# Performance work log

Measured on AMD Instinct MI355X. Metric: run time of the kernel, lower is better.

The kernel has to match this reference:

```python
import jax, jax.numpy as jnp
import numpy as np

N, T, D, H = 8192, 60, 6, 64  # stocks, lookback, d_feat, hidden_size
NEG_SLOPE = 0.01


def setup_inputs() -> dict:
    key = jax.random.key(0)
    ks = jax.random.split(key, 16)
    s = 0.1
    inp = {
        "x": jax.random.normal(ks[0], (N, D * T), jnp.float32),
        # GRU layer 0 (input D -> H), PyTorch gate order [r, z, n]
        "gru_Wih0": jax.random.normal(ks[1], (3 * H, D), jnp.float32) * s,
        "gru_Whh0": jax.random.normal(ks[2], (3 * H, H), jnp.float32) * s,
        "gru_bih0": jax.random.normal(ks[3], (3 * H,), jnp.float32) * s,
        "gru_bhh0": jax.random.normal(ks[4], (3 * H,), jnp.float32) * s,
        # GRU layer 1 (H -> H)
        "gru_Wih1": jax.random.normal(ks[5], (3 * H, H), jnp.float32) * s,
        "gru_Whh1": jax.random.normal(ks[6], (3 * H, H), jnp.float32) * s,
        "gru_bih1": jax.random.normal(ks[7], (3 * H,), jnp.float32) * s,
        "gru_bhh1": jax.random.normal(ks[8], (3 * H,), jnp.float32) * s,
        # attention head
        "transfer_W": jax.random.normal(ks[9], (H, H), jnp.float32) * s,
        "transfer_b": jax.random.normal(ks[10], (H,), jnp.float32) * s,
        "a": jax.random.normal(ks[11], (2 * H, 1), jnp.float32) * s,
        # output head
        "fc_W": jax.random.normal(ks[12], (H, H), jnp.float32) * s,
        "fc_b": jax.random.normal(ks[13], (H,), jnp.float32) * s,
        "out_W": jax.random.normal(ks[14], (1, H), jnp.float32) * s,
        "out_b": jax.random.normal(ks[15], (1,), jnp.float32) * s,
    }
    return inp


def _gru_layer(xs, Wih, Whh, bih, bhh):
    # xs: [T, N, in]; PyTorch GRU cell math, gate order r,z,n
    Hs = Whh.shape[1]

    def step(h, xt):
        gi = xt @ Wih.T + bih
        gh = h @ Whh.T + bhh
        ir, iz, inn = jnp.split(gi, 3, axis=-1)
        hr, hz, hn = jnp.split(gh, 3, axis=-1)
        r = jax.nn.sigmoid(ir + hr)
        z = jax.nn.sigmoid(iz + hz)
        n = jnp.tanh(inn + r * hn)
        h_new = (1.0 - z) * n + z * h
        return h_new, h_new

    h0 = jnp.zeros((xs.shape[1], Hs), xs.dtype)
    _, ys = jax.lax.scan(step, h0, xs)
    return ys  # [T, N, Hs]


def reference(x, gru_Wih0, gru_Whh0, gru_bih0, gru_bhh0,
              gru_Wih1, gru_Whh1, gru_bih1, gru_bhh1,
              transfer_W, transfer_b, a, fc_W, fc_b, out_W, out_b):
    # [N, D*T] -> [N, D, T] -> [T, N, D]
    xs = jnp.transpose(x.reshape(x.shape[0], D, -1), (2, 0, 1))
    ys0 = _gru_layer(xs, gru_Wih0, gru_Whh0, gru_bih0, gru_bhh0)
    ys1 = _gru_layer(ys0, gru_Wih1, gru_Whh1, gru_bih1, gru_bhh1)
    hidden = ys1[-1]  # [N, H] == out[:, -1, :]

    # self_attention: score[k, i] = a[:H].(W x_i) + a[H:].(W x_k)
    t = hidden @ transfer_W.T + transfer_b
    a1 = a[:H, 0]
    a2 = a[H:, 0]
    s1 = t @ a1  # contribution of column index i
    s2 = t @ a2  # contribution of row index k
    scores = jax.nn.leaky_relu(s2[:, None] + s1[None, :], NEG_SLOPE)  # [N, N]
    att = jax.nn.softmax(scores, axis=1)

    h = att @ hidden + hidden
    h = jax.nn.leaky_relu(h @ fc_W.T + fc_b, NEG_SLOPE)
    return (h @ out_W.T + out_b).squeeze()
```

## Files before the change

### kernel.cpp

```cpp
#include <hip/hip_runtime.h>
#include <hip/hip_bf16.h>
#include <math.h>

#define TSTEPS 60
#define DIN 6

typedef __attribute__((ext_vector_type(8))) short short8v;
typedef __attribute__((ext_vector_type(4))) float f32x4;
#define MFMA16 __builtin_amdgcn_mfma_f32_16x16x32_bf16

__device__ __forceinline__ float fast_rcp(float x) { return __builtin_amdgcn_rcpf(x); }
__device__ __forceinline__ float sigf(float x) { return fast_rcp(1.0f + __expf(-x)); }
__device__ __forceinline__ float tanhf_(float x) {
    return 1.0f - 2.0f * fast_rcp(__expf(2.0f * x) + 1.0f);
}
__device__ __forceinline__ unsigned short f2bf(float f) {
    unsigned u = __float_as_uint(f);
    u += 0x7fff + ((u >> 16) & 1);
    return (unsigned short)(u >> 16);
}
__device__ __forceinline__ float bf2f(unsigned short s) {
    return __uint_as_float(((unsigned)s) << 16);
}

__global__ __launch_bounds__(512, 1)
void gru_fused(const float* __restrict__ x,
               const float* __restrict__ Wih0, const float* __restrict__ Whh0,
               const float* __restrict__ bih0, const float* __restrict__ bhh0,
               const float* __restrict__ Wih1, const float* __restrict__ Whh1,
               const float* __restrict__ bih1, const float* __restrict__ bhh1,
               float* __restrict__ hidden)
{
    extern __shared__ char ldsb[];
    const int W0H = 0, W0L = 24576, W1IH = 49152, W1IL = 73728,
              W1HH = 98304, W1HL = 122880, HP = 147456;

    const int tid = threadIdx.x;
    const int l   = tid & 63;
    const int w   = tid >> 6;
    const int mt  = w >> 2;
    const int ur  = w & 3;
    const int l15 = l & 15;
    const int kb  = l >> 4;
    const int u_m = ur * 16 + l15;
    const int n0  = blockIdx.x * 32;

    for (int i = tid; i < 12288; i += 512) {
        int u = i >> 6, j = i & 63;
        int off = u * 128 + (((j >> 3) ^ (u & 7)) << 4) + (j & 7) * 2;
        float w0 = Whh0[i], w1 = Wih1[i], w2 = Whh1[i];
        unsigned short h0 = f2bf(w0); unsigned short l0 = f2bf(w0 - bf2f(h0));
        unsigned short h1 = f2bf(w1); unsigned short l1 = f2bf(w1 - bf2f(h1));
        unsigned short h2 = f2bf(w2); unsigned short l2 = f2bf(w2 - bf2f(h2));
        *(unsigned short*)(ldsb + W0H  + off) = h0;
        *(unsigned short*)(ldsb + W0L  + off) = l0;
        *(unsigned short*)(ldsb + W1IH + off) = h1;
        *(unsigned short*)(ldsb + W1IL + off) = l1;
        *(unsigned short*)(ldsb + W1HH + off) = h2;
        *(unsigned short*)(ldsb + W1HL + off) = l2;
    }
    for (int i = tid; i < 4096; i += 512) *(unsigned*)(ldsb + HP + i * 4) = 0u;

    float brz0_r = bih0[u_m] + bhh0[u_m];
    float brz0_z = bih0[64 + u_m] + bhh0[64 + u_m];
    float bi0n = bih0[128 + u_m], bh0n = bhh0[128 + u_m];
    float brz1_r = bih1[u_m] + bhh1[u_m];
    float brz1_z = bih1[64 + u_m] + bhh1[64 + u_m];
    float bi1n = bih1[128 + u_m], bh1n = bhh1[128 + u_m];

    float Wx[3][DIN];
#pragma unroll
    for (int g = 0; g < 3; ++g)
#pragma unroll
        for (int d = 0; d < DIN; ++d) Wx[g][d] = Wih0[(g * 64 + u_m) * DIN + d];

    const int rowA = mt * 16 + l15;
    const int bA0 = HP + rowA * 128 + ((kb ^ (rowA & 7)) << 4);
    const int bA1 = bA0 ^ 64;
    const int bB0 = u_m * 128 + ((kb ^ (u_m & 7)) << 4);
    const int bB1 = bB0 ^ 64;
    int wAo[4];
#pragma unroll
    for (int i = 0; i < 4; ++i) {
        int r = mt * 16 + kb * 4 + i;
        wAo[i] = HP + r * 128 + ((((u_m >> 3) & 7) ^ (r & 7)) << 4) + (u_m & 7) * 2;
    }
    const float* xp[4];
#pragma unroll
    for (int i = 0; i < 4; ++i)
        xp[i] = x + (size_t)(n0 + mt * 16 + kb * 4 + i) * (DIN * TSTEPS);

    float h0f[4] = {0.f, 0.f, 0.f, 0.f};
    float h1f[4] = {0.f, 0.f, 0.f, 0.f};

    __syncthreads();

#define LD8(o) (*(const short8v*)(ldsb + (o)))

    short8v B0[3][2][2];
#pragma unroll
    for (int g = 0; g < 3; ++g) {
        B0[g][0][0] = LD8(W0H + g * 8192 + bB0);
        B0[g][0][1] = LD8(W0H + g * 8192 + bB1);
        B0[g][1][0] = LD8(W0L + g * 8192 + bB0);
        B0[g][1][1] = LD8(W0L + g * 8192 + bB1);
    }

#pragma unroll 1
    for (int t = 0; t < TSTEPS; ++t) {
        float xv[4][DIN];
#pragma unroll
        for (int i = 0; i < 4; ++i)
#pragma unroll
            for (int d = 0; d < DIN; ++d) xv[i][d] = xp[i][d * TSTEPS + t];

        short8v aH0[2][2], aH1[2][2];
        aH0[0][0] = LD8(bA0);        aH0[1][0] = LD8(bA1);
        aH0[0][1] = LD8(bA0 + 4096); aH0[1][1] = LD8(bA1 + 4096);
        aH1[0][0] = LD8(bA0 + 8192); aH1[1][0] = LD8(bA1 + 8192);
        aH1[0][1] = LD8(bA0 + 12288); aH1[1][1] = LD8(bA1 + 12288);

        float gi0[4], gi1[4], gi2[4];
#pragma unroll
        for (int i = 0; i < 4; ++i) {
            float s0 = 0.f, s1 = 0.f, s2 = 0.f;
#pragma unroll
            for (int d = 0; d < DIN; ++d) {
                float xd = xv[i][d];
                s0 = fmaf(Wx[0][d], xd, s0);
                s1 = fmaf(Wx[1][d], xd, s1);
                s2 = fmaf(Wx[2][d], xd, s2);
            }
            gi0[i] = s0; gi1[i] = s1; gi2[i] = s2;
        }

        f32x4 Cr, Cz, Cnh;
#pragma unroll
        for (int i = 0; i < 4; ++i) {
            Cr[i] = brz0_r + gi0[i]; Cz[i] = brz0_z + gi1[i]; Cnh[i] = bh0n;
        }
        Cr = MFMA16(aH0[0][0], B0[0][0][0], Cr, 0, 0, 0);
        Cr = MFMA16(aH0[1][0], B0[0][0][1], Cr, 0, 0, 0);
        Cr = MFMA16(aH0[0][1], B0[0][0][0], Cr, 0, 0, 0);
        Cr = MFMA16(aH0[1][1], B0[0][0][1], Cr, 0, 0, 0);
        Cr = MFMA16(aH0[0][0], B0[0][1][0], Cr, 0, 0, 0);
        Cr = MFMA16(aH0[1][0], B0[0][1][1], Cr, 0, 0, 0);
        Cz = MFMA16(aH0[0][0], B0[1][0][0], Cz, 0, 0, 0);
        Cz = MFMA16(aH0[1][0], B0[1][0][1], Cz, 0, 0, 0);
        Cz = MFMA16(aH0[0][1], B0[1][0][0], Cz, 0, 0, 0);
        Cz = MFMA16(aH0[1][1], B0[1][0][1], Cz, 0, 0, 0);
        Cz = MFMA16(aH0[0][0], B0[1][1][0], Cz, 0, 0, 0);
        Cz = MFMA16(aH0[1][0], B0[1][1][1], Cz, 0, 0, 0);
        Cnh = MFMA16(aH0[0][0], B0[2][0][0], Cnh, 0, 0, 0);
        Cnh = MFMA16(aH0[1][0], B0[2][0][1], Cnh, 0, 0, 0);
        Cnh = MFMA16(aH0[0][1], B0[2][0][0], Cnh, 0, 0, 0);
        Cnh = MFMA16(aH0[1][1], B0[2][0][1], Cnh, 0, 0, 0);
        Cnh = MFMA16(aH0[0][0], B0[2][1][0], Cnh, 0, 0, 0);
        Cnh = MFMA16(aH0[1][0], B0[2][1][1], Cnh, 0, 0, 0);

        unsigned short hh[4], hl[4];
#pragma unroll
        for (int i = 0; i < 4; ++i) {
            float r = sigf(Cr[i]);
            float z = sigf(Cz[i]);
            float n = tanhf_(gi2[i] + bi0n + r * Cnh[i]);
            h0f[i] = (1.f - z) * n + z * h0f[i];
            hh[i] = f2bf(h0f[i]);
            hl[i] = f2bf(h0f[i] - bf2f(hh[i]));
        }
        __syncthreads();
#pragma unroll
        for (int i = 0; i < 4; ++i) {
            *(unsigned short*)(ldsb + wAo[i]) = hh[i];
            *(unsigned short*)(ldsb + wAo[i] + 4096) = hl[i];
        }
        __syncthreads();

        short8v aN[2][2];
        aN[0][0] = LD8(bA0);        aN[1][0] = LD8(bA1);
        aN[0][1] = LD8(bA0 + 4096); aN[1][1] = LD8(bA1 + 4096);

        f32x4 Dr, Dz, Dni, Dnh;
#pragma unroll
        for (int i = 0; i < 4; ++i) {
            Dr[i] = brz1_r; Dz[i] = brz1_z; Dni[i] = bi1n; Dnh[i] = bh1n;
        }
        {
            short8v bih_ = LD8(W1IH + bB0), bih1_ = LD8(W1IH + bB1);
            short8v bil_ = LD8(W1IL + bB0), bil1_ = LD8(W1IL + bB1);
            Dr = MFMA16(aN[0][0], bih_, Dr, 0, 0, 0);
            Dr = MFMA16(aN[1][0], bih1_, Dr, 0, 0, 0);
            Dr = MFMA16(aN[0][1], bih_, Dr, 0, 0, 0);
            Dr = MFMA16(aN[1][1], bih1_, Dr, 0, 0, 0);
            Dr = MFMA16(aN[0][0], bil_, Dr, 0, 0, 0);
            Dr = MFMA16(aN[1][0], bil1_, Dr, 0, 0, 0);
            short8v bhh_ = LD8(W1HH + bB0), bhh1_ = LD8(W1HH + bB1);
            short8v bhl_ = LD8(W1HL + bB0), bhl1_ = LD8(W1HL + bB1);
            Dr = MFMA16(aH1[0][0], bhh_, Dr, 0, 0, 0);
            Dr = MFMA16(aH1[1][0], bhh1_, Dr, 0, 0, 0);
            Dr = MFMA16(aH1[0][1], bhh_, Dr, 0, 0, 0);
            Dr = MFMA16(aH1[1][1], bhh1_, Dr, 0, 0, 0);
            Dr = MFMA16(aH1[0][0], bhl_, Dr, 0, 0, 0);
            Dr = MFMA16(aH1[1][0], bhl1_, Dr, 0, 0, 0);
        }
        {
            short8v bih_ = LD8(W1IH + 8192 + bB0), bih1_ = LD8(W1IH + 8192 + bB1);
            short8v bil_ = LD8(W1IL + 8192 + bB0), bil1_ = LD8(W1IL + 8192 + bB1);
            Dz = MFMA16(aN[0][0], bih_, Dz, 0, 0, 0);
            Dz = MFMA16(aN[1][0], bih1_, Dz, 0, 0, 0);
            Dz = MFMA16(aN[0][1], bih_, Dz, 0, 0, 0);
            Dz = MFMA16(aN[1][1], bih1_, Dz, 0, 0, 0);
            Dz = MFMA16(aN[0][0], bil_, Dz, 0, 0, 0);
            Dz = MFMA16(aN[1][0], bil1_, Dz, 0, 0, 0);
            short8v bhh_ = LD8(W1HH + 8192 + bB0), bhh1_ = LD8(W1HH + 8192 + bB1);
            short8v bhl_ = LD8(W1HL + 8192 + bB0), bhl1_ = LD8(W1HL + 8192 + bB1);
            Dz = MFMA16(aH1[0][0], bhh_, Dz, 0, 0, 0);
            Dz = MFMA16(aH1[1][0], bhh1_, Dz, 0, 0, 0);
            Dz = MFMA16(aH1[0][1], bhh_, Dz, 0, 0, 0);
            Dz = MFMA16(aH1[1][1], bhh1_, Dz, 0, 0, 0);
            Dz = MFMA16(aH1[0][0], bhl_, Dz, 0, 0, 0);
            Dz = MFMA16(aH1[1][0], bhl1_, Dz, 0, 0, 0);
        }
        {
            short8v bih_ = LD8(W1IH + 16384 + bB0), bih1_ = LD8(W1IH + 16384 + bB1);
            short8v bil_ = LD8(W1IL + 16384 + bB0), bil1_ = LD8(W1IL + 16384 + bB1);
            Dni = MFMA16(aN[0][0], bih_, Dni, 0, 0, 0);
            Dni = MFMA16(aN[1][0], bih1_, Dni, 0, 0, 0);
            Dni = MFMA16(aN[0][1], bih_, Dni, 0, 0, 0);
            Dni = MFMA16(aN[1][1], bih1_, Dni, 0, 0, 0);
            Dni = MFMA16(aN[0][0], bil_, Dni, 0, 0, 0);
            Dni = MFMA16(aN[1][0], bil1_, Dni, 0, 0, 0);
            short8v bhh_ = LD8(W1HH + 16384 + bB0), bhh1_ = LD8(W1HH + 16384 + bB1);
            short8v bhl_ = LD8(W1HL + 16384 + bB0), bhl1_ = LD8(W1HL + 16384 + bB1);
            Dnh = MFMA16(aH1[0][0], bhh_, Dnh, 0, 0, 0);
            Dnh = MFMA16(aH1[1][0], bhh1_, Dnh, 0, 0, 0);
            Dnh = MFMA16(aH1[0][1], bhh_, Dnh, 0, 0, 0);
            Dnh = MFMA16(aH1[1][1], bhh1_, Dnh, 0, 0, 0);
            Dnh = MFMA16(aH1[0][0], bhl_, Dnh, 0, 0, 0);
            Dnh = MFMA16(aH1[1][0], bhl1_, Dnh, 0, 0, 0);
        }
#pragma unroll
        for (int i = 0; i < 4; ++i) {
            float r = sigf(Dr[i]);
            float z = sigf(Dz[i]);
            float n = tanhf_(Dni[i] + r * Dnh[i]);
            h1f[i] = (1.f - z) * n + z * h1f[i];
            unsigned short hhi = f2bf(h1f[i]);
            *(unsigned short*)(ldsb + wAo[i] + 8192) = hhi;
            *(unsigned short*)(ldsb + wAo[i] + 12288) = f2bf(h1f[i] - bf2f(hhi));
        }
        __syncthreads();
    }

#pragma unroll
    for (int i = 0; i < 4; ++i)
        hidden[(size_t)(n0 + mt * 16 + kb * 4 + i) * 64 + u_m] = h1f[i];
#undef LD8
}

__global__ __launch_bounds__(256)
void attn_prep(const float* __restrict__ hidden, const float* __restrict__ tW,
               const float* __restrict__ tb, const float* __restrict__ a,
               float* __restrict__ s1, float* __restrict__ s2,
               float* __restrict__ E1p, float* __restrict__ E1n,
               float* __restrict__ E2p, float* __restrict__ E2n)
{
    __shared__ float WT[64 * 64];
    __shared__ float hrow[4][64];
    int tid = threadIdx.x, c = tid & 63, rw = tid >> 6;
    for (int i = tid; i < 4096; i += 256) WT[i] = tW[(i & 63) * 64 + (i >> 6)];
    int row = blockIdx.x * 4 + rw;
    hrow[rw][c] = hidden[(size_t)row * 64 + c];
    __syncthreads();
    float tc = tb[c];
    for (int u = 0; u < 64; ++u) tc += WT[u * 64 + c] * hrow[rw][u];
    float p1 = tc * a[c], p2 = tc * a[64 + c];
#pragma unroll
    for (int o = 32; o; o >>= 1) { p1 += __shfl_xor(p1, o); p2 += __shfl_xor(p2, o); }
    if (c == 0) {
        s1[row] = p1; s2[row] = p2;
        E1p[row] = expf(p1); E1n[row] = expf(0.01f * p1);
        E2p[row] = expf(p2); E2n[row] = expf(0.01f * p2);
    }
}

__global__ __launch_bounds__(256)
void transposeHbf(const float* __restrict__ hidden,
                  unsigned short* __restrict__ hiTh, unsigned short* __restrict__ hiTl)
{
    __shared__ float tile[64][65];
    int b = blockIdx.x, tid = threadIdx.x;
    for (int i = tid; i < 4096; i += 256) {
        int r = i >> 6, c = i & 63;
        tile[c][r] = hidden[(size_t)(b * 64 + r) * 64 + c];
    }
    __syncthreads();
    int c = tid & 63, seg = tid >> 6;
    unsigned short oh[16], ol[16];
#pragma unroll
    for (int k = 0; k < 16; ++k) {
        float v = tile[c][seg * 16 + k];
        unsigned short h = f2bf(v);
        oh[k] = h; ol[k] = f2bf(v - bf2f(h));
    }
    size_t base = (size_t)c * 8192 + b * 64 + seg * 16;
    *(short8v*)(hiTh + base)     = *(const short8v*)(oh);
    *(short8v*)(hiTh + base + 8) = *(const short8v*)(oh + 8);
    *(short8v*)(hiTl + base)     = *(const short8v*)(ol);
    *(short8v*)(hiTl + base + 8) = *(const short8v*)(ol + 8);
}

__global__ __launch_bounds__(256)
void flash_attn(const float* __restrict__ s1, const float* __restrict__ s2,
                const float* __restrict__ E1p, const float* __restrict__ E1n,
                const float* __restrict__ E2p, const float* __restrict__ E2n,
                const unsigned short* __restrict__ hiTh,
                const unsigned short* __restrict__ hiTl,
                const float* __restrict__ hidden, float* __restrict__ h2)
{
    __shared__ float comb[4][64][17];
    const int tid = threadIdx.x;
    const int l = tid & 63, w = tid >> 6;
    const int iw = w >> 1, jh = w & 1;
    const int l15 = l & 15, kb = l >> 4;
    const int i0 = blockIdx.x * 32 + iw * 16;

    const float s2i  = s2[i0 + l15];
    const float E2pv = E2p[i0 + l15];
    const float E2nv = E2n[i0 + l15];

    f32x4 C[4];
#pragma unroll
    for (int ct = 0; ct < 4; ++ct)
#pragma unroll
        for (int r = 0; r < 4; ++r) C[ct][r] = 0.f;
    float den = 0.f;

#pragma unroll 2
    for (int it = 0; it < 128; ++it) {
        const int jk = jh * 4096 + it * 32 + kb * 8;
        float4 s1a = *(const float4*)(s1 + jk);
        float4 s1b = *(const float4*)(s1 + jk + 4);
        float4 p1a = *(const float4*)(E1p + jk);
        float4 p1b = *(const float4*)(E1p + jk + 4);
        float4 n1a = *(const float4*)(E1n + jk);
        float4 n1b = *(const float4*)(E1n + jk + 4);

        short8v Bh[4], Bl[4];
#pragma unroll
        for (int ct = 0; ct < 4; ++ct) {
            size_t off = (size_t)(ct * 16 + l15) * 8192 + jk;
            Bh[ct] = *(const short8v*)(hiTh + off);
            Bl[ct] = *(const short8v*)(hiTl + off);
        }

        unsigned short ah[8], al[8];
#define MK(e, sv, pv, nv)                                            \
        {                                                            \
            float s = s2i + (sv);                                    \
            bool cpos = s > 0.f;                                     \
            float w1 = cpos ? (pv) : (nv);                           \
            float w2 = cpos ? E2pv : E2nv;                           \
            float ev = w1 * w2;                                      \
            den += ev;                                               \
            unsigned short hx = f2bf(ev);                            \
            ah[e] = hx; al[e] = f2bf(ev - bf2f(hx));                 \
        }
        MK(0, s1a.x, p1a.x, n1a.x) MK(1, s1a.y, p1a.y, n1a.y)
        MK(2, s1a.z, p1a.z, n1a.z) MK(3, s1a.w, p1a.w, n1a.w)
        MK(4, s1b.x, p1b.x, n1b.x) MK(5, s1b.y, p1b.y, n1b.y)
        MK(6, s1b.z, p1b.z, n1b.z) MK(7, s1b.w, p1b.w, n1b.w)
#undef MK
        short8v Ah = { (short)ah[0], (short)ah[1], (short)ah[2], (short)ah[3],
                       (short)ah[4], (short)ah[5], (short)ah[6], (short)ah[7] };
        short8v Al = { (short)al[0], (short)al[1], (short)al[2], (short)al[3],
                       (short)al[4], (short)al[5], (short)al[6], (short)al[7] };

#pragma unroll
        for (int ct = 0; ct < 4; ++ct) {
            C[ct] = MFMA16(Ah, Bh[ct], C[ct], 0, 0, 0);
            C[ct] = MFMA16(Al, Bh[ct], C[ct], 0, 0, 0);
            C[ct] = MFMA16(Ah, Bl[ct], C[ct], 0, 0, 0);
        }
    }

    den += __shfl_xor(den, 16);
    den += __shfl_xor(den, 32);

#pragma unroll
    for (int ct = 0; ct < 4; ++ct)
#pragma unroll
        for (int r = 0; r < 4; ++r) comb[w][l][ct * 4 + r] = C[ct][r];
    comb[w][l][16] = den;
    __syncthreads();

    if (jh == 0) {
        float den_t = comb[w][l][16] + comb[w + 1][l][16];
#pragma unroll
        for (int ct = 0; ct < 4; ++ct) {
#pragma unroll
            for (int r = 0; r < 4; ++r) {
                int rr = kb * 4 + r;
                float num = comb[w][l][ct * 4 + r] + comb[w + 1][l][ct * 4 + r];
                float dv = __shfl(den_t, rr);
                size_t oidx = (size_t)(i0 + rr) * 64 + ct * 16 + l15;
                h2[oidx] = num / dv + hidden[oidx];
            }
        }
    }
}

__global__ __launch_bounds__(256)
void fc_out(const float* __restrict__ h2,
            const float* __restrict__ fcW, const float* __restrict__ fcb,
            const float* __restrict__ outW, const float* __restrict__ outb,
            float* __restrict__ out)
{
    __shared__ float fcWT[64 * 64];
    __shared__ float hrow[4][64];
    int tid = threadIdx.x, c = tid & 63, rw = tid >> 6;
    for (int i = tid; i < 4096; i += 256) fcWT[i] = fcW[(i & 63) * 64 + (i >> 6)];
    int row = blockIdx.x * 4 + rw;
    hrow[rw][c] = h2[(size_t)row * 64 + c];
    __syncthreads();
    float y = fcb[c];
    for (int u = 0; u < 64; ++u) y += fcWT[u * 64 + c] * hrow[rw][u];
    y = y > 0.f ? y : 0.01f * y;
    float o = y * outW[c];
#pragma unroll
    for (int s = 32; s; s >>= 1) o += __shfl_xor(o, s);
    if (c == 0) out[row] = o + outb[0];
}

extern "C" void kernel_launch(void* const* d_in, const int* in_sizes, int n_in,
                              void* d_out, int out_size, void* d_ws, size_t ws_size,
                              hipStream_t stream)
{
    const float* x     = (const float*)d_in[0];
    const float* Wih0  = (const float*)d_in[1];
    const float* Whh0  = (const float*)d_in[2];
    const float* bih0  = (const float*)d_in[3];
    const float* bhh0  = (const float*)d_in[4];
    const float* Wih1  = (const float*)d_in[5];
    const float* Whh1  = (const float*)d_in[6];
    const float* bih1  = (const float*)d_in[7];
    const float* bhh1  = (const float*)d_in[8];
    const float* tW    = (const float*)d_in[9];
    const float* tb    = (const float*)d_in[10];
    const float* a     = (const float*)d_in[11];
    const float* fcW   = (const float*)d_in[12];
    const float* fcb   = (const float*)d_in[13];
    const float* outW  = (const float*)d_in[14];
    const float* outb  = (const float*)d_in[15];

    float* ws      = (float*)d_ws;
    float* hidden  = ws;
    float* s1      = hidden + 524288;
    float* s2      = s1 + 8192;
    float* E1p     = s2 + 8192;
    float* E1n     = E1p + 8192;
    float* E2p     = E1n + 8192;
    float* E2n     = E2p + 8192;
    unsigned short* hiTh = (unsigned short*)(ws + 573440);
    unsigned short* hiTl = hiTh + 524288;
    float* h2      = ws + 573440 + 524288;

    hipStreamCaptureStatus cap = hipStreamCaptureStatusNone;
    hipStreamIsCapturing(stream, &cap);
    if (cap == hipStreamCaptureStatusNone) {
        hipFuncSetAttribute(reinterpret_cast<const void*>(gru_fused),
                            hipFuncAttributeMaxDynamicSharedMemorySize, 163840);
    }

    gru_fused<<<256, 512, 163840, stream>>>(x, Wih0, Whh0, bih0, bhh0,
                                            Wih1, Whh1, bih1, bhh1, hidden);
    attn_prep<<<2048, 256, 0, stream>>>(hidden, tW, tb, a, s1, s2,
                                        E1p, E1n, E2p, E2n);
    transposeHbf<<<128, 256, 0, stream>>>(hidden, hiTh, hiTl);
    flash_attn<<<256, 256, 0, stream>>>(s1, s2, E1p, E1n, E2p, E2n,
                                        hiTh, hiTl, hidden, h2);
    fc_out<<<2048, 256, 0, stream>>>(h2, fcW, fcb, outW, outb, (float*)d_out);
}
```

Baseline: 433.1 us.

## Keep GRU weights in registers, shrink LDS, re-tile attention and fix bank conflicts

The GRU kernel now loads its recurrent and layer-1 input weights straight into registers as split bf16 hi/lo fragments instead of staging them in 160KB of LDS. Only the 16KB hidden-state buffer stays in shared memory, so two blocks can share a CU, and the per-step LDS weight reads go away. The flash attention kernel is re-tiled to 16 rows per block over 512 blocks, with the key dimension split across four waves and a blocked transposed-hidden layout that gives contiguous loads. The transposed weight tables in attn_prep and fc_out are padded to a stride of 65 to avoid bank conflicts. The catch is much higher register pressure in the GRU kernel, which could spill or fail to reach the intended occupancy.

```diff
diff --git a/kernel.cpp b/kernel.cpp
--- a/kernel.cpp
+++ b/kernel.cpp
@@ -22,8 +22,19 @@
 __device__ __forceinline__ float bf2f(unsigned short s) {
     return __uint_as_float(((unsigned)s) << 16);
 }
-
-__global__ __launch_bounds__(512, 1)
+__device__ __forceinline__ void ld_split(const float* p, short8v& hi, short8v& lo) {
+    float4 a = *(const float4*)p, b = *(const float4*)(p + 4);
+    float v[8] = {a.x, a.y, a.z, a.w, b.x, b.y, b.z, b.w};
+    short h8[8], l8[8];
+#pragma unroll
+    for (int e = 0; e < 8; ++e) {
+        unsigned short h = f2bf(v[e]);
+        h8[e] = (short)h; l8[e] = (short)f2bf(v[e] - bf2f(h));
+    }
+    hi = *(short8v*)h8; lo = *(short8v*)l8;
+}
+
+__global__ __launch_bounds__(512, 2)
 void gru_fused(const float* __restrict__ x,
                const float* __restrict__ Wih0, const float* __restrict__ Whh0,
                const float* __restrict__ bih0, const float* __restrict__ bhh0,
@@ -31,9 +42,7 @@
                const float* __restrict__ bih1, const float* __restrict__ bhh1,
                float* __restrict__ hidden)
 {
-    extern __shared__ char ldsb[];
-    const int W0H = 0, W0L = 24576, W1IH = 49152, W1IL = 73728,
-              W1HH = 98304, W1HL = 122880, HP = 147456;
+    __shared__ char ldsb[16384];
 
     const int tid = threadIdx.x;
     const int l   = tid & 63;
@@ -45,21 +54,20 @@
     const int u_m = ur * 16 + l15;
     const int n0  = blockIdx.x * 32;
 
-    for (int i = tid; i < 12288; i += 512) {
-        int u = i >> 6, j = i & 63;
-        int off = u * 128 + (((j >> 3) ^ (u & 7)) << 4) + (j & 7) * 2;
-        float w0 = Whh0[i], w1 = Wih1[i], w2 = Whh1[i];
-        unsigned short h0 = f2bf(w0); unsigned short l0 = f2bf(w0 - bf2f(h0));
-        unsigned short h1 = f2bf(w1); unsigned short l1 = f2bf(w1 - bf2f(h1));
-        unsigned short h2 = f2bf(w2); unsigned short l2 = f2bf(w2 - bf2f(h2));
-        *(unsigned short*)(ldsb + W0H  + off) = h0;
-        *(unsigned short*)(ldsb + W0L  + off) = l0;
-        *(unsigned short*)(ldsb + W1IH + off) = h1;
-        *(unsigned short*)(ldsb + W1IL + off) = l1;
-        *(unsigned short*)(ldsb + W1HH + off) = h2;
-        *(unsigned short*)(ldsb + W1HL + off) = l2;
-    }
-    for (int i = tid; i < 4096; i += 512) *(unsigned*)(ldsb + HP + i * 4) = 0u;
+    for (int i = tid; i < 4096; i += 512) *(unsigned*)(ldsb + i * 4) = 0u;
+
+    short8v W0h[3][2], W0l[3][2];
+    short8v V1h[3][2], V1l[3][2];
+    short8v U1h[3][2], U1l[3][2];
+#pragma unroll
+    for (int g = 0; g < 3; ++g)
+#pragma unroll
+        for (int kt = 0; kt < 2; ++kt) {
+            int off = (g * 64 + u_m) * 64 + kt * 32 + kb * 8;
+            ld_split(Whh0 + off, W0h[g][kt], W0l[g][kt]);
+            ld_split(Wih1 + off, V1h[g][kt], V1l[g][kt]);
+            ld_split(Whh1 + off, U1h[g][kt], U1l[g][kt]);
+        }
 
     float brz0_r = bih0[u_m] + bhh0[u_m];
     float brz0_z = bih0[64 + u_m] + bhh0[64 + u_m];
@@ -75,15 +83,13 @@
         for (int d = 0; d < DIN; ++d) Wx[g][d] = Wih0[(g * 64 + u_m) * DIN + d];
 
     const int rowA = mt * 16 + l15;
-    const int bA0 = HP + rowA * 128 + ((kb ^ (rowA & 7)) << 4);
+    const int bA0 = rowA * 128 + ((kb ^ (rowA & 7)) << 4);
     const int bA1 = bA0 ^ 64;
-    const int bB0 = u_m * 128 + ((kb ^ (u_m & 7)) << 4);
-    const int bB1 = bB0 ^ 64;
     int wAo[4];
 #pragma unroll
     for (int i = 0; i < 4; ++i) {
         int r = mt * 16 + kb * 4 + i;
-        wAo[i] = HP + r * 128 + ((((u_m >> 3) & 7) ^ (r & 7)) << 4) + (u_m & 7) * 2;
+        wAo[i] = r * 128 + (((u_m >> 3) ^ (r & 7)) << 4) + (u_m & 7) * 2;
     }
     const float* xp[4];
 #pragma unroll
@@ -97,73 +103,54 @@
 
 #define LD8(o) (*(const short8v*)(ldsb + (o)))
 
-    short8v B0[3][2][2];
-#pragma unroll
-    for (int g = 0; g < 3; ++g) {
-        B0[g][0][0] = LD8(W0H + g * 8192 + bB0);
-        B0[g][0][1] = LD8(W0H + g * 8192 + bB1);
-        B0[g][1][0] = LD8(W0L + g * 8192 + bB0);
-        B0[g][1][1] = LD8(W0L + g * 8192 + bB1);
-    }
-
 #pragma unroll 1
     for (int t = 0; t < TSTEPS; ++t) {
-        float xv[4][DIN];
-#pragma unroll
-        for (int i = 0; i < 4; ++i)
-#pragma unroll
-            for (int d = 0; d < DIN; ++d) xv[i][d] = xp[i][d * TSTEPS + t];
-
-        short8v aH0[2][2], aH1[2][2];
+        short8v aH0[2][2];
         aH0[0][0] = LD8(bA0);        aH0[1][0] = LD8(bA1);
         aH0[0][1] = LD8(bA0 + 4096); aH0[1][1] = LD8(bA1 + 4096);
-        aH1[0][0] = LD8(bA0 + 8192); aH1[1][0] = LD8(bA1 + 8192);
-        aH1[0][1] = LD8(bA0 + 12288); aH1[1][1] = LD8(bA1 + 12288);
-
-        float gi0[4], gi1[4], gi2[4];
+
+        f32x4 Cr, Cz, Cnh;
 #pragma unroll
         for (int i = 0; i < 4; ++i) {
-            float s0 = 0.f, s1 = 0.f, s2 = 0.f;
+            float s0 = brz0_r, s1 = brz0_z, s2 = 0.f;
 #pragma unroll
             for (int d = 0; d < DIN; ++d) {
-                float xd = xv[i][d];
+                float xd = xp[i][d * TSTEPS + t];
                 s0 = fmaf(Wx[0][d], xd, s0);
                 s1 = fmaf(Wx[1][d], xd, s1);
                 s2 = fmaf(Wx[2][d], xd, s2);
             }
-            gi0[i] = s0; gi1[i] = s1; gi2[i] = s2;
-        }
-
-        f32x4 Cr, Cz, Cnh;
-#pragma unroll
-        for (int i = 0; i < 4; ++i) {
-            Cr[i] = brz0_r + gi0[i]; Cz[i] = brz0_z + gi1[i]; Cnh[i] = bh0n;
-        }
-        Cr = MFMA16(aH0[0][0], B0[0][0][0], Cr, 0, 0, 0);
-        Cr = MFMA16(aH0[1][0], B0[0][0][1], Cr, 0, 0, 0);
-        Cr = MFMA16(aH0[0][1], B0[0][0][0], Cr, 0, 0, 0);
-        Cr = MFMA16(aH0[1][1], B0[0][0][1], Cr, 0, 0, 0);
-        Cr = MFMA16(aH0[0][0], B0[0][1][0], Cr, 0, 0, 0);
-        Cr = MFMA16(aH0[1][0], B0[0][1][1], Cr, 0, 0, 0);
-        Cz = MFMA16(aH0[0][0], B0[1][0][0], Cz, 0, 0, 0);
-        Cz = MFMA16(aH0[1][0], B0[1][0][1], Cz, 0, 0, 0);
-        Cz = MFMA16(aH0[0][1], B0[1][0][0], Cz, 0, 0, 0);
-        Cz = MFMA16(aH0[1][1], B0[1][0][1], Cz, 0, 0, 0);
-        Cz = MFMA16(aH0[0][0], B0[1][1][0], Cz, 0, 0, 0);
-        Cz = MFMA16(aH0[1][0], B0[1][1][1], Cz, 0, 0, 0);
-        Cnh = MFMA16(aH0[0][0], B0[2][0][0], Cnh, 0, 0, 0);
-        Cnh = MFMA16(aH0[1][0], B0[2][0][1], Cnh, 0, 0, 0);
-        Cnh = MFMA16(aH0[0][1], B0[2][0][0], Cnh, 0, 0, 0);
-        Cnh = MFMA16(aH0[1][1], B0[2][0][1], Cnh, 0, 0, 0);
-        Cnh = MFMA16(aH0[0][0], B0[2][1][0], Cnh, 0, 0, 0);
-        Cnh = MFMA16(aH0[1][0], B0[2][1][1], Cnh, 0, 0, 0);
+            Cr[i] = s0; Cz[i] = s1; Cnh[i] = s2;
+        }
+        float gin[4];
+#pragma unroll
+        for (int i = 0; i < 4; ++i) { gin[i] = Cnh[i]; Cnh[i] = bh0n; }
+
+        Cr = MFMA16(aH0[0][0], W0h[0][0], Cr, 0, 0, 0);
+        Cr = MFMA16(aH0[1][0], W0h[0][1], Cr, 0, 0, 0);
+        Cr = MFMA16(aH0[0][1], W0h[0][0], Cr, 0, 0, 0);
+        Cr = MFMA16(aH0[1][1], W0h[0][1], Cr, 0, 0, 0);
+        Cr = MFMA16(aH0[0][0], W0l[0][0], Cr, 0, 0, 0);
+        Cr = MFMA16(aH0[1][0], W0l[0][1], Cr, 0, 0, 0);
+        Cz = MFMA16(aH0[0][0], W0h[1][0], Cz, 0, 0, 0);
+        Cz = MFMA16(aH0[1][0], W0h[1][1], Cz, 0, 0, 0);
+        Cz = MFMA16(aH0[0][1], W0h[1][0], Cz, 0, 0, 0);
+        Cz = MFMA16(aH0[1][1], W0h[1][1], Cz, 0, 0, 0);
+        Cz = MFMA16(aH0[0][0], W0l[1][0], Cz, 0, 0, 0);
+        Cz = MFMA16(aH0[1][0], W0l[1][1], Cz, 0, 0, 0);
+        Cnh = MFMA16(aH0[0][0], W0h[2][0], Cnh, 0, 0, 0);
+        Cnh = MFMA16(aH0[1][0], W0h[2][1], Cnh, 0, 0, 0);
+        Cnh = MFMA16(aH0[0][1], W0h[2][0], Cnh, 0, 0, 0);
+        Cnh = MFMA16(aH0[1][1], W0h[2][1], Cnh, 0, 0, 0);
+        Cnh = MFMA16(aH0[0][0], W0l[2][0], Cnh, 0, 0, 0);
+        Cnh = MFMA16(aH0[1][0], W0l[2][1], Cnh, 0, 0, 0);
 
         unsigned short hh[4], hl[4];
 #pragma unroll
         for (int i = 0; i < 4; ++i) {
             float r = sigf(Cr[i]);
             float z = sigf(Cz[i]);
-            float n = tanhf_(gi2[i] + bi0n + r * Cnh[i]);
+            float n = tanhf_(gin[i] + bi0n + r * Cnh[i]);
             h0f[i] = (1.f - z) * n + z * h0f[i];
             hh[i] = f2bf(h0f[i]);
             hl[i] = f2bf(h0f[i] - bf2f(hh[i]));
@@ -174,6 +161,9 @@
             *(unsigned short*)(ldsb + wAo[i]) = hh[i];
             *(unsigned short*)(ldsb + wAo[i] + 4096) = hl[i];
         }
+        short8v aH1[2][2];
+        aH1[0][0] = LD8(bA0 + 8192);  aH1[1][0] = LD8(bA1 + 8192);
+        aH1[0][1] = LD8(bA0 + 12288); aH1[1][1] = LD8(bA1 + 12288);
         __syncthreads();
 
         short8v aN[2][2];
@@ -185,60 +175,45 @@
         for (int i = 0; i < 4; ++i) {
             Dr[i] = brz1_r; Dz[i] = brz1_z; Dni[i] = bi1n; Dnh[i] = bh1n;
         }
-        {
-            short8v bih_ = LD8(W1IH + bB0), bih1_ = LD8(W1IH + bB1);
-            short8v bil_ = LD8(W1IL + bB0), bil1_ = LD8(W1IL + bB1);
-            Dr = MFMA16(aN[0][0], bih_, Dr, 0, 0, 0);
-            Dr = MFMA16(aN[1][0], bih1_, Dr, 0, 0, 0);
-            Dr = MFMA16(aN[0][1], bih_, Dr, 0, 0, 0);
-            Dr = MFMA16(aN[1][1], bih1_, Dr, 0, 0, 0);
-            Dr = MFMA16(aN[0][0], bil_, Dr, 0, 0, 0);
-            Dr = MFMA16(aN[1][0], bil1_, Dr, 0, 0, 0);
-            short8v bhh_ = LD8(W1HH + bB0), bhh1_ = LD8(W1HH + bB1);
-            short8v bhl_ = LD8(W1HL + bB0), bhl1_ = LD8(W1HL + bB1);
-            Dr = MFMA16(aH1[0][0], bhh_, Dr, 0, 0, 0);
-            Dr = MFMA16(aH1[1][0], bhh1_, Dr, 0, 0, 0);
-            Dr = MFMA16(aH1[0][1], bhh_, Dr, 0, 0, 0);
-            Dr = MFMA16(aH1[1][1], bhh1_, Dr, 0, 0, 0);
-            Dr = MFMA16(aH1[0][0], bhl_, Dr, 0, 0, 0);
-            Dr = MFMA16(aH1[1][0], bhl1_, Dr, 0, 0, 0);
-        }
-        {
-            short8v bih_ = LD8(W1IH + 8192 + bB0), bih1_ = LD8(W1IH + 8192 + bB1);
-            short8v bil_ = LD8(W1IL + 8192 + bB0), bil1_ = LD8(W1IL + 8192 + bB1);
-            Dz = MFMA16(aN[0][0], bih_, Dz, 0, 0, 0);
-            Dz = MFMA16(aN[1][0], bih1_, Dz, 0, 0, 0);
-            Dz = MFMA16(aN[0][1], bih_, Dz, 0, 0, 0);
-            Dz = MFMA16(aN[1][1], bih1_, Dz, 0, 0, 0);
-            Dz = MFMA16(aN[0][0], bil_, Dz, 0, 0, 0);
-            Dz = MFMA16(aN[1][0], bil1_, Dz, 0, 0, 0);
-            short8v bhh_ = LD8(W1HH + 8192 + bB0), bhh1_ = LD8(W1HH + 8192 + bB1);
-            short8v bhl_ = LD8(W1HL + 8192 + bB0), bhl1_ = LD8(W1HL + 8192 + bB1);
-            Dz = MFMA16(aH1[0][0], bhh_, Dz, 0, 0, 0);
-            Dz = MFMA16(aH1[1][0], bhh1_, Dz, 0, 0, 0);
-            Dz = MFMA16(aH1[0][1], bhh_, Dz, 0, 0, 0);
-            Dz = MFMA16(aH1[1][1], bhh1_, Dz, 0, 0, 0);
-            Dz = MFMA16(aH1[0][0], bhl_, Dz, 0, 0, 0);
-            Dz = MFMA16(aH1[1][0], bhl1_, Dz, 0, 0, 0);
-        }
-        {
-            short8v bih_ = LD8(W1IH + 16384 + bB0), bih1_ = LD8(W1IH + 16384 + bB1);
-            short8v bil_ = LD8(W1IL + 16384 + bB0), bil1_ = LD8(W1IL + 16384 + bB1);
-            Dni = MFMA16(aN[0][0], bih_, Dni, 0, 0, 0);
-            Dni = MFMA16(aN[1][0], bih1_, Dni, 0, 0, 0);
-            Dni = MFMA16(aN[0][1], bih_, Dni, 0, 0, 0);
-            Dni = MFMA16(aN[1][1], bih1_, Dni, 0, 0, 0);
-            Dni = MFMA16(aN[0][0], bil_, Dni, 0, 0, 0);
-            Dni = MFMA16(aN[1][0], bil1_, Dni, 0, 0, 0);
-            short8v bhh_ = LD8(W1HH + 16384 + bB0), bhh1_ = LD8(W1HH + 16384 + bB1);
-            short8v bhl_ = LD8(W1HL + 16384 + bB0), bhl1_ = LD8(W1HL + 16384 + bB1);
-            Dnh = MFMA16(aH1[0][0], bhh_, Dnh, 0, 0, 0);
-            Dnh = MFMA16(aH1[1][0], bhh1_, Dnh, 0, 0, 0);
-            Dnh = MFMA16(aH1[0][1], bhh_, Dnh, 0, 0, 0);
-            Dnh = MFMA16(aH1[1][1], bhh1_, Dnh, 0, 0, 0);
-            Dnh = MFMA16(aH1[0][0], bhl_, Dnh, 0, 0, 0);
-            Dnh = MFMA16(aH1[1][0], bhl1_, Dnh, 0, 0, 0);
-        }
+        Dr = MFMA16(aN[0][0], V1h[0][0], Dr, 0, 0, 0);
+        Dr = MFMA16(aN[1][0], V1h[0][1], Dr, 0, 0, 0);
+        Dr = MFMA16(aN[0][1], V1h[0][0], Dr, 0, 0, 0);
+        Dr = MFMA16(aN[1][1], V1h[0][1], Dr, 0, 0, 0);
+        Dr = MFMA16(aN[0][0], V1l[0][0], Dr, 0, 0, 0);
+        Dr = MFMA16(aN[1][0], V1l[0][1], Dr, 0, 0, 0);
+        Dr = MFMA16(aH1[0][0], U1h[0][0], Dr, 0, 0, 0);
+        Dr = MFMA16(aH1[1][0], U1h[0][1], Dr, 0, 0, 0);
+        Dr = MFMA16(aH1[0][1], U1h[0][0], Dr, 0, 0, 0);
+        Dr = MFMA16(aH1[1][1], U1h[0][1], Dr, 0, 0, 0);
+        Dr = MFMA16(aH1[0][0], U1l[0][0], Dr, 0, 0, 0);
+        Dr = MFMA16(aH1[1][0], U1l[0][1], Dr, 0, 0, 0);
+
+        Dz = MFMA16(aN[0][0], V1h[1][0], Dz, 0, 0, 0);
+        Dz = MFMA16(aN[1][0], V1h[1][1], Dz, 0, 0, 0);
+        Dz = MFMA16(aN[0][1], V1h[1][0], Dz, 0, 0, 0);
+        Dz = MFMA16(aN[1][1], V1h[1][1], Dz, 0, 0, 0);
+        Dz = MFMA16(aN[0][0], V1l[1][0], Dz, 0, 0, 0);
+        Dz = MFMA16(aN[1][0], V1l[1][1], Dz, 0, 0, 0);
+        Dz = MFMA16(aH1[0][0], U1h[1][0], Dz, 0, 0, 0);
+        Dz = MFMA16(aH1[1][0], U1h[1][1], Dz, 0, 0, 0);
+        Dz = MFMA16(aH1[0][1], U1h[1][0], Dz, 0, 0, 0);
+        Dz = MFMA16(aH1[1][1], U1h[1][1], Dz, 0, 0, 0);
+        Dz = MFMA16(aH1[0][0], U1l[1][0], Dz, 0, 0, 0);
+        Dz = MFMA16(aH1[1][0], U1l[1][1], Dz, 0, 0, 0);
+
+        Dni = MFMA16(aN[0][0], V1h[2][0], Dni, 0, 0, 0);
+        Dni = MFMA16(aN[1][0], V1h[2][1], Dni, 0, 0, 0);
+        Dni = MFMA16(aN[0][1], V1h[2][0], Dni, 0, 0, 0);
+        Dni = MFMA16(aN[1][1], V1h[2][1], Dni, 0, 0, 0);
+        Dni = MFMA16(aN[0][0], V1l[2][0], Dni, 0, 0, 0);
+        Dni = MFMA16(aN[1][0], V1l[2][1], Dni, 0, 0, 0);
+        Dnh = MFMA16(aH1[0][0], U1h[2][0], Dnh, 0, 0, 0);
+        Dnh = MFMA16(aH1[1][0], U1h[2][1], Dnh, 0, 0, 0);
+        Dnh = MFMA16(aH1[0][1], U1h[2][0], Dnh, 0, 0, 0);
+        Dnh = MFMA16(aH1[1][1], U1h[2][1], Dnh, 0, 0, 0);
+        Dnh = MFMA16(aH1[0][0], U1l[2][0], Dnh, 0, 0, 0);
+        Dnh = MFMA16(aH1[1][0], U1l[2][1], Dnh, 0, 0, 0);
+
 #pragma unroll
         for (int i = 0; i < 4; ++i) {
             float r = sigf(Dr[i]);
@@ -265,15 +240,18 @@
                float* __restrict__ E1p, float* __restrict__ E1n,
                float* __restrict__ E2p, float* __restrict__ E2n)
 {
-    __shared__ float WT[64 * 64];
+    __shared__ float WT[64 * 65];
     __shared__ float hrow[4][64];
     int tid = threadIdx.x, c = tid & 63, rw = tid >> 6;
-    for (int i = tid; i < 4096; i += 256) WT[i] = tW[(i & 63) * 64 + (i >> 6)];
+    for (int i = tid; i < 4096; i += 256) {
+        int cc = i >> 6, u = i & 63;
+        WT[u * 65 + cc] = tW[i];
+    }
     int row = blockIdx.x * 4 + rw;
     hrow[rw][c] = hidden[(size_t)row * 64 + c];
     __syncthreads();
     float tc = tb[c];
-    for (int u = 0; u < 64; ++u) tc += WT[u * 64 + c] * hrow[rw][u];
+    for (int u = 0; u < 64; ++u) tc += WT[u * 65 + c] * hrow[rw][u];
     float p1 = tc * a[c], p2 = tc * a[64 + c];
 #pragma unroll
     for (int o = 32; o; o >>= 1) { p1 += __shfl_xor(p1, o); p2 += __shfl_xor(p2, o); }
@@ -303,11 +281,13 @@
         unsigned short h = f2bf(v);
         oh[k] = h; ol[k] = f2bf(v - bf2f(h));
     }
-    size_t base = (size_t)c * 8192 + b * 64 + seg * 16;
-    *(short8v*)(hiTh + base)     = *(const short8v*)(oh);
-    *(short8v*)(hiTh + base + 8) = *(const short8v*)(oh + 8);
-    *(short8v*)(hiTl + base)     = *(const short8v*)(ol);
-    *(short8v*)(hiTl + base + 8) = *(const short8v*)(ol + 8);
+    int jb = b * 8 + seg * 2;
+    size_t b0 = ((size_t)jb * 64 + c) * 8;
+    size_t b1 = ((size_t)(jb + 1) * 64 + c) * 8;
+    *(short8v*)(hiTh + b0) = *(const short8v*)(oh);
+    *(short8v*)(hiTh + b1) = *(const short8v*)(oh + 8);
+    *(short8v*)(hiTl + b0) = *(const short8v*)(ol);
+    *(short8v*)(hiTl + b1) = *(const short8v*)(ol + 8);
 }
 
 __global__ __launch_bounds__(256)
@@ -321,9 +301,8 @@
     __shared__ float comb[4][64][17];
     const int tid = threadIdx.x;
     const int l = tid & 63, w = tid >> 6;
-    const int iw = w >> 1, jh = w & 1;
     const int l15 = l & 15, kb = l >> 4;
-    const int i0 = blockIdx.x * 32 + iw * 16;
+    const int i0 = blockIdx.x * 16;
 
     const float s2i  = s2[i0 + l15];
     const float E2pv = E2p[i0 + l15];
@@ -337,8 +316,9 @@
     float den = 0.f;
 
 #pragma unroll 2
-    for (int it = 0; it < 128; ++it) {
-        const int jk = jh * 4096 + it * 32 + kb * 8;
+    for (int it = 0; it < 64; ++it) {
+        const int jk = w * 2048 + it * 32 + kb * 8;
+        const int jb = w * 256 + it * 4 + kb;
         float4 s1a = *(const float4*)(s1 + jk);
         float4 s1b = *(const float4*)(s1 + jk + 4);
         float4 p1a = *(const float4*)(E1p + jk);
@@ -349,7 +329,7 @@
         short8v Bh[4], Bl[4];
 #pragma unroll
         for (int ct = 0; ct < 4; ++ct) {
-            size_t off = (size_t)(ct * 16 + l15) * 8192 + jk;
+            size_t off = ((size_t)jb * 64 + ct * 16 + l15) * 8;
             Bh[ct] = *(const short8v*)(hiTh + off);
             Bl[ct] = *(const short8v*)(hiTl + off);
         }
@@ -394,14 +374,15 @@
     comb[w][l][16] = den;
     __syncthreads();
 
-    if (jh == 0) {
-        float den_t = comb[w][l][16] + comb[w + 1][l][16];
+    if (w == 0) {
+        float den_t = comb[0][l][16] + comb[1][l][16] + comb[2][l][16] + comb[3][l][16];
 #pragma unroll
         for (int ct = 0; ct < 4; ++ct) {
 #pragma unroll
             for (int r = 0; r < 4; ++r) {
                 int rr = kb * 4 + r;
-                float num = comb[w][l][ct * 4 + r] + comb[w + 1][l][ct * 4 + r];
+                float num = comb[0][l][ct * 4 + r] + comb[1][l][ct * 4 + r]
+                          + comb[2][l][ct * 4 + r] + comb[3][l][ct * 4 + r];
                 float dv = __shfl(den_t, rr);
                 size_t oidx = (size_t)(i0 + rr) * 64 + ct * 16 + l15;
                 h2[oidx] = num / dv + hidden[oidx];
@@ -416,15 +397,18 @@
             const float* __restrict__ outW, const float* __restrict__ outb,
             float* __restrict__ out)
 {
-    __shared__ float fcWT[64 * 64];
+    __shared__ float fcWT[64 * 65];
     __shared__ float hrow[4][64];
     int tid = threadIdx.x, c = tid & 63, rw = tid >> 6;
-    for (int i = tid; i < 4096; i += 256) fcWT[i] = fcW[(i & 63) * 64 + (i >> 6)];
+    for (int i = tid; i < 4096; i += 256) {
+        int cc = i >> 6, u = i & 63;
+        fcWT[u * 65 + cc] = fcW[i];
+    }
     int row = blockIdx.x * 4 + rw;
     hrow[rw][c] = h2[(size_t)row * 64 + c];
     __syncthreads();
     float y = fcb[c];
-    for (int u = 0; u < 64; ++u) y += fcWT[u * 64 + c] * hrow[rw][u];
+    for (int u = 0; u < 64; ++u) y += fcWT[u * 65 + c] * hrow[rw][u];
     y = y > 0.f ? y : 0.01f * y;
     float o = y * outW[c];
 #pragma unroll
@@ -465,19 +449,12 @@
     unsigned short* hiTl = hiTh + 524288;
     float* h2      = ws + 573440 + 524288;
 
-    hipStreamCaptureStatus cap = hipStreamCaptureStatusNone;
-    hipStreamIsCapturing(stream, &cap);
-    if (cap == hipStreamCaptureStatusNone) {
-        hipFuncSetAttribute(reinterpret_cast<const void*>(gru_fused),
-                            hipFuncAttributeMaxDynamicSharedMemorySize, 163840);
-    }
-
-    gru_fused<<<256, 512, 163840, stream>>>(x, Wih0, Whh0, bih0, bhh0,
-                                            Wih1, Whh1, bih1, bhh1, hidden);
+    gru_fused<<<256, 512, 0, stream>>>(x, Wih0, Whh0, bih0, bhh0,
+                                       Wih1, Whh1, bih1, bhh1, hidden);
     attn_prep<<<2048, 256, 0, stream>>>(hidden, tW, tb, a, s1, s2,
                                         E1p, E1n, E2p, E2n);
     transposeHbf<<<128, 256, 0, stream>>>(hidden, hiTh, hiTl);
-    flash_attn<<<256, 256, 0, stream>>>(s1, s2, E1p, E1n, E2p, E2n,
+    flash_attn<<<512, 256, 0, stream>>>(s1, s2, E1p, E1n, E2p, E2n,
                                         hiTh, hiTl, hidden, h2);
     fc_out<<<2048, 256, 0, stream>>>(h2, fcW, fcb, outW, outb, (float*)d_out);
 }
```

New measurement: 568.2 us. 1.31x slower.
